# Kernel tuning notes

Measured on AMD Instinct MI355X. Metric: run time of the kernel, lower is better.

Reference implementation:

```python
import jax, jax.numpy as jnp
import numpy as np

M = 16                      # multiplicity of each irrep block
INV3 = 1.0 / np.sqrt(3.0)   # w3j(1,1,0) component-normalized
INV2 = 1.0 / np.sqrt(2.0)   # w3j(1,1,1) component-normalized
A0 = 1.0 / np.sqrt(2.0 * M) # fan-in norm for 0e outputs (2 paths x mul 16)
A1 = 1.0 / np.sqrt(3.0 * M) # fan-in norm for 1o outputs (3 paths x mul 16)


def setup_inputs() -> dict:
    E, N, ED, HID = 100000, 10000, 32, 128
    WNUM = 2 * M * (2 * M) + 3 * M * M  # 1792 per-edge TP weights
    ks = jax.random.split(jax.random.key(0), 10)
    return {
        "dst": jax.random.randint(ks[0], (E,), 0, N),
        "x_src": jax.random.normal(ks[1], (E, 4 * M), jnp.float32),   # 16x0e+16x1o
        "x_dst": jax.random.normal(ks[2], (N, 4 * M), jnp.float32),
        "sh": jax.random.normal(ks[3], (E, 4), jnp.float32),          # 1x0e+1x1o
        "edge_attr": jax.random.normal(ks[4], (E, ED), jnp.float32),
        "We1": jax.random.normal(ks[5], (ED, HID), jnp.float32) / np.sqrt(ED),
        "be1": jnp.zeros((HID,), jnp.float32),
        "We2": jax.random.normal(ks[6], (HID, WNUM), jnp.float32) / np.sqrt(HID),
        "be2": jnp.zeros((WNUM,), jnp.float32),
        "Wr0": jax.random.normal(ks[7], (M, 2 * M), jnp.float32),     # 16x0e -> 32x0e
        "Wr1": jax.random.normal(ks[8], (M, M), jnp.float32),         # 16x1o -> 16x1o
    }


def _forward(dst, x_src, x_dst, sh, edge_attr, We1, be1, We2, be2, Wr0, Wr1):
    E = x_src.shape[0]
    N = x_dst.shape[0]
    o0 = 2 * M  # 32x0e tp output (scalars + gates)

    # edge MLP -> per-edge tensor-product weights [E, 1792]
    w = jax.nn.relu(edge_attr @ We1 + be1) @ We2 + be2
    i = 0
    w_ss = w[:, i:i + M * o0].reshape(E, M, o0); i += M * o0   # 0e x 0e -> 0e
    w_vv0 = w[:, i:i + M * o0].reshape(E, M, o0); i += M * o0  # 1o x 1o -> 0e
    w_sv = w[:, i:i + M * M].reshape(E, M, M); i += M * M      # 0e x 1o -> 1o
    w_vs = w[:, i:i + M * M].reshape(E, M, M); i += M * M      # 1o x 0e -> 1o
    w_vv1 = w[:, i:i + M * M].reshape(E, M, M)                 # 1o x 1o -> 1o

    s1 = x_src[:, :M]                       # [E, 16]
    v1 = x_src[:, M:].reshape(E, M, 3)      # [E, 16, 3]
    s2 = sh[:, 0]                           # [E]
    v2 = sh[:, 1:4]                         # [E, 3]

    # fully-connected tensor product with per-edge weights
    out0 = A0 * (jnp.einsum('em,emo->eo', s1 * s2[:, None], w_ss)
                 + INV3 * jnp.einsum('emc,ec,emo->eo', v1, v2, w_vv0))  # [E, 32]
    cross = jnp.cross(v1, v2[:, None, :])   # [E, 16, 3]
    out1 = A1 * (jnp.einsum('em,ec,emo->eoc', s1, v2, w_sv)
                 + jnp.einsum('emc,e,emo->eoc', v1, s2, w_vs)
                 + INV2 * jnp.einsum('emc,emo->eoc', cross, w_vv1))     # [E, 16, 3]
    msg = jnp.concatenate([out0, out1.reshape(E, -1)], axis=1)          # [E, 80]

    # scatter-mean over destination nodes
    ssum = jax.ops.segment_sum(msg, dst, num_segments=N)
    cnt = jax.ops.segment_sum(jnp.ones((E,), msg.dtype), dst, num_segments=N)
    msg = ssum / jnp.maximum(cnt, 1.0)[:, None]                          # [N, 80]

    # residual equivariant linear on x_dst
    sd = x_dst[:, :M]
    vd = x_dst[:, M:].reshape(N, M, 3)
    res0 = (sd @ Wr0) / np.sqrt(M)                                       # [N, 32]
    res1 = jnp.einsum('nmc,mo->noc', vd, Wr1) / np.sqrt(M)               # [N, 16, 3]
    msg = msg + jnp.concatenate([res0, res1.reshape(N, -1)], axis=1)

    # gate nonlinearity: relu(scalars), sigmoid(gates) * gated vectors
    scalars = jax.nn.relu(msg[:, :M])
    gates = jax.nn.sigmoid(msg[:, M:2 * M])
    gated = msg[:, 2 * M:].reshape(N, M, 3) * gates[:, :, None]
    return jnp.concatenate([scalars, gated.reshape(N, -1)], axis=1)      # [N, 64]


def reference(dst, x_src, x_dst, sh, edge_attr, We1, be1, We2, be2, Wr0, Wr1):
    return _forward(dst, x_src, x_dst, sh, edge_attr, We1, be1, We2, be2, Wr0, Wr1)
```

## Files before the change

### kernel.cpp

```cpp
#include <hip/hip_runtime.h>
#include <math.h>

#define WNUM 1792
#define HID 128

#define INV3C 0.5773502691896258f
#define INV2C 0.7071067811865476f
#define A0C   0.17677669529663687f
#define A1C   0.14433756729740643f
#define MAXDEG 64

typedef short bf8 __attribute__((ext_vector_type(8)));
typedef _Float16 f16x8 __attribute__((ext_vector_type(8)));
typedef _Float16 f16x4 __attribute__((ext_vector_type(4)));
typedef float f32x4 __attribute__((ext_vector_type(4)));

__device__ inline unsigned short f2bf(float f) {
  union { float f; unsigned u; } v; v.f = f;
  unsigned r = v.u + 0x7FFFu + ((v.u >> 16) & 1u);
  return (unsigned short)(r >> 16);
}
__device__ inline float bf2f(unsigned short h) {
  union { unsigned u; float f; } v; v.u = ((unsigned)h) << 16;
  return v.f;
}
__device__ inline float wscale(int t) {
  if (t < 32) return A0C;
  if (t < 64) return A0C * INV3C;
  if (t < 96) return A1C;
  return A1C * INV2C;
}

__global__ __launch_bounds__(256) void prep_kernel(
    const float* __restrict__ We1, const float* __restrict__ We2,
    const float* __restrict__ be2,
    unsigned short* __restrict__ we1x, _Float16* __restrict__ we2h,
    float* __restrict__ be2p, int* __restrict__ cntp, int N)
{
  int i = blockIdx.x * 256 + threadIdx.x;
  if (i < 28672) {
    int t = i >> 8, c = (i >> 6) & 3, lane = i & 63;
    int quad = lane >> 4, l15 = lane & 15;
    int col = t * 16 + l15;
    float sc = wscale(t);
    f16x8 v;
    #pragma unroll
    for (int j = 0; j < 8; ++j) {
      int k = c * 32 + quad * 8 + j;
      v[j] = (_Float16)(We2[(size_t)k * WNUM + col] * sc);
    }
    *(f16x8*)(we2h + (size_t)t * 2048 + c * 512 + lane * 8) = v;
  } else if (i < 29184) {
    int q = i - 28672;
    int c1 = q >> 6, lane = q & 63;
    int quad = lane >> 4, l15 = lane & 15;
    int col = c1 * 16 + l15;
    bf8 hh, ll;
    #pragma unroll
    for (int j = 0; j < 8; ++j) {
      int k = quad * 8 + j;
      float v = We1[k * HID + col];
      unsigned short hi = f2bf(v);
      hh[j] = (short)hi;
      ll[j] = (short)f2bf(v - bf2f(hi));
    }
    *(bf8*)(we1x + c1 * 1024 + lane * 8) = hh;
    *(bf8*)(we1x + c1 * 1024 + 512 + lane * 8) = ll;
  } else if (i < 30976) {
    int q = i - 29184;
    int t = q >> 4, l16 = q & 15;
    be2p[(t >> 1) * 32 + l16 * 2 + (t & 1)] = be2[q] * wscale(t);
  } else if (i < 30976 + N) {
    cntp[i - 30976] = 0;
  }
}

__device__ inline void chains2(const f16x8* a0, const f16x8* a1,
    f16x8 b0, f16x8 b1, f16x8 b2, f16x8 b3,
    f16x8 b4, f16x8 b5, f16x8 b6, f16x8 b7,
    float2 bias, f32x4* wa, f32x4* wb)
{
  f32x4 ca0 = {bias.x, bias.x, bias.x, bias.x};
  f32x4 cb0 = {bias.y, bias.y, bias.y, bias.y};
  f32x4 ca1 = ca0, cb1 = cb0;
  ca0 = __builtin_amdgcn_mfma_f32_16x16x32_f16(a0[0], b0, ca0, 0, 0, 0);
  cb0 = __builtin_amdgcn_mfma_f32_16x16x32_f16(a0[0], b4, cb0, 0, 0, 0);
  ca1 = __builtin_amdgcn_mfma_f32_16x16x32_f16(a1[0], b0, ca1, 0, 0, 0);
  cb1 = __builtin_amdgcn_mfma_f32_16x16x32_f16(a1[0], b4, cb1, 0, 0, 0);
  ca0 = __builtin_amdgcn_mfma_f32_16x16x32_f16(a0[1], b1, ca0, 0, 0, 0);
  cb0 = __builtin_amdgcn_mfma_f32_16x16x32_f16(a0[1], b5, cb0, 0, 0, 0);
  ca1 = __builtin_amdgcn_mfma_f32_16x16x32_f16(a1[1], b1, ca1, 0, 0, 0);
  cb1 = __builtin_amdgcn_mfma_f32_16x16x32_f16(a1[1], b5, cb1, 0, 0, 0);
  ca0 = __builtin_amdgcn_mfma_f32_16x16x32_f16(a0[2], b2, ca0, 0, 0, 0);
  cb0 = __builtin_amdgcn_mfma_f32_16x16x32_f16(a0[2], b6, cb0, 0, 0, 0);
  ca1 = __builtin_amdgcn_mfma_f32_16x16x32_f16(a1[2], b2, ca1, 0, 0, 0);
  cb1 = __builtin_amdgcn_mfma_f32_16x16x32_f16(a1[2], b6, cb1, 0, 0, 0);
  ca0 = __builtin_amdgcn_mfma_f32_16x16x32_f16(a0[3], b3, ca0, 0, 0, 0);
  cb0 = __builtin_amdgcn_mfma_f32_16x16x32_f16(a0[3], b7, cb0, 0, 0, 0);
  ca1 = __builtin_amdgcn_mfma_f32_16x16x32_f16(a1[3], b3, ca1, 0, 0, 0);
  cb1 = __builtin_amdgcn_mfma_f32_16x16x32_f16(a1[3], b7, cb1, 0, 0, 0);
  wa[0] = ca0; wb[0] = cb0; wa[1] = ca1; wb[1] = cb1;
}

__device__ inline void pair_mm(const _Float16* bL, const float* bp, int p,
                               const f16x8 (&af)[2][4], f32x4* wa, f32x4* wb)
{
  f16x8 b0 = *(const f16x8*)(bL);
  f16x8 b1 = *(const f16x8*)(bL + 512);
  f16x8 b2 = *(const f16x8*)(bL + 1024);
  f16x8 b3 = *(const f16x8*)(bL + 1536);
  f16x8 b4 = *(const f16x8*)(bL + 2048);
  f16x8 b5 = *(const f16x8*)(bL + 2560);
  f16x8 b6 = *(const f16x8*)(bL + 3072);
  f16x8 b7 = *(const f16x8*)(bL + 3584);
  float2 bias2 = *(const float2*)(bp + p * 32);
  chains2(af[0], af[1], b0, b1, b2, b3, b4, b5, b6, b7, bias2, wa, wb);
}

template <bool MSG>
__global__ __launch_bounds__(256, 2) void edge_kernel(
    const float* __restrict__ ea, const float* __restrict__ xsrc,
    const float* __restrict__ sh, const int* __restrict__ dst,
    const float* __restrict__ be1,
    const unsigned short* __restrict__ we1x, const _Float16* __restrict__ we2h,
    const float* __restrict__ be2p,
    float* __restrict__ outp, int* __restrict__ eidx, int* __restrict__ cntp, int E)
{
  const int lane = threadIdx.x & 63;
  const int w    = threadIdx.x >> 6;
  const int quad = lane >> 4;
  const int l16  = lane & 15;
  const int eb   = (blockIdx.x * 4 + w) * 32;

  __shared__ union SMem {
    _Float16 h[4][32][136];
    _Float16 B[4][4096];
  } uS;
  __shared__ _Float16 fss_s[4][16][32];
  __shared__ _Float16 fvv_s[4][16][32];
  __shared__ _Float16 s1h_s[4][16][32];
  __shared__ _Float16 v1h_s[4][16][3][32];
  __shared__ float4 vq_s[4][32];

  #define STAGE_PAIR(p) { \
    const _Float16* gsrc_ = we2h + (size_t)(p) * 4096; \
    _Float16* ldst_ = &uS.B[(p) & 3][0]; \
    __builtin_amdgcn_global_load_lds( \
      (const __attribute__((address_space(1))) void*)(gsrc_ + (w * 2) * 512 + lane * 8), \
      (__attribute__((address_space(3))) void*)(ldst_ + (w * 2) * 512), 16, 0, 0); \
    __builtin_amdgcn_global_load_lds( \
      (const __attribute__((address_space(1))) void*)(gsrc_ + (w * 2 + 1) * 512 + lane * 8), \
      (__attribute__((address_space(3))) void*)(ldst_ + (w * 2 + 1) * 512), 16, 0, 0); \
  }

  if (lane < 32) {
    int ge = eb + lane;
    if (ge < E) {
      int node = dst[ge];
      int pos = atomicAdd(cntp + node, 1);
      if (MSG) { if (pos < MAXDEG) eidx[node * MAXDEG + pos] = ge; }
    }
  }

  {
    int e2 = lane >> 1, mg = lane & 1;
    int ge = eb + e2;
    if (ge < E) {
      const float* xp = xsrc + (size_t)ge * 64;
      float4 sq0 = *(const float4*)(xp + mg * 8);
      float4 sq1 = *(const float4*)(xp + mg * 8 + 4);
      float s1a[8] = {sq0.x,sq0.y,sq0.z,sq0.w,sq1.x,sq1.y,sq1.z,sq1.w};
      const float* vp = xp + 16 + mg * 24;
      float la[24];
      #pragma unroll
      for (int qv = 0; qv < 6; ++qv) {
        float4 t = *(const float4*)(vp + qv * 4);
        la[qv*4+0] = t.x; la[qv*4+1] = t.y; la[qv*4+2] = t.z; la[qv*4+3] = t.w;
      }
      float4 shq = *(const float4*)(sh + (size_t)ge * 4);
      float s2 = shq.x, v2x = shq.y, v2y = shq.z, v2z = shq.w;
      #pragma unroll
      for (int mi = 0; mi < 8; ++mi) {
        int m = mg * 8 + mi;
        float v1x = la[mi*3], v1y = la[mi*3+1], v1z = la[mi*3+2];
        fss_s[w][m][e2] = (_Float16)(s1a[mi] * s2);
        fvv_s[w][m][e2] = (_Float16)(v1x*v2x + v1y*v2y + v1z*v2z);
        s1h_s[w][m][e2] = (_Float16)s1a[mi];
        v1h_s[w][m][0][e2] = (_Float16)v1x;
        v1h_s[w][m][1][e2] = (_Float16)v1y;
        v1h_s[w][m][2][e2] = (_Float16)v1z;
      }
      if (mg == 0) vq_s[w][e2] = make_float4(v2x, v2y, v2z, s2);
    } else {
      #pragma unroll
      for (int mi = 0; mi < 8; ++mi) {
        int m = mg * 8 + mi;
        fss_s[w][m][e2] = (_Float16)0.f;
        fvv_s[w][m][e2] = (_Float16)0.f;
        s1h_s[w][m][e2] = (_Float16)0.f;
        v1h_s[w][m][0][e2] = (_Float16)0.f;
        v1h_s[w][m][1][e2] = (_Float16)0.f;
        v1h_s[w][m][2][e2] = (_Float16)0.f;
      }
      if (mg == 0) vq_s[w][e2] = make_float4(0,0,0,0);
    }
  }

  {
    bf8 ah[2], al[2];
    #pragma unroll
    for (int g = 0; g < 2; ++g) {
      int gea = eb + g * 16 + l16; if (gea > E - 1) gea = E - 1;
      const float* ep = ea + (size_t)gea * 32 + quad * 8;
      float4 p0 = *(const float4*)ep;
      float4 p1 = *(const float4*)(ep + 4);
      float pv[8] = {p0.x,p0.y,p0.z,p0.w,p1.x,p1.y,p1.z,p1.w};
      #pragma unroll
      for (int j = 0; j < 8; ++j) {
        unsigned short hi = f2bf(pv[j]);
        ah[g][j] = (short)hi;
        al[g][j] = (short)f2bf(pv[j] - bf2f(hi));
      }
    }
    const unsigned short* wb1 = we1x + lane * 8;
    #pragma unroll 2
    for (int c = 0; c < 8; ++c) {
      bf8 bh = *(const bf8*)(wb1 + c * 1024);
      bf8 bl = *(const bf8*)(wb1 + c * 1024 + 512);
      float bias = be1[c * 16 + l16];
      #pragma unroll
      for (int g = 0; g < 2; ++g) {
        f32x4 hc = {bias, bias, bias, bias};
        hc = __builtin_amdgcn_mfma_f32_16x16x32_bf16(al[g], bh, hc, 0, 0, 0);
        hc = __builtin_amdgcn_mfma_f32_16x16x32_bf16(ah[g], bl, hc, 0, 0, 0);
        hc = __builtin_amdgcn_mfma_f32_16x16x32_bf16(ah[g], bh, hc, 0, 0, 0);
        #pragma unroll
        for (int r = 0; r < 4; ++r)
          uS.h[w][g * 16 + quad * 4 + r][c * 16 + l16] = (_Float16)fmaxf(hc[r], 0.f);
      }
    }
  }
  __syncthreads();

  f16x8 af[2][4];
  #pragma unroll
  for (int g = 0; g < 2; ++g)
    #pragma unroll
    for (int ch = 0; ch < 4; ++ch)
      af[g][ch] = *(const f16x8*)&uS.h[w][g * 16 + l16][ch * 32 + quad * 8];
  __syncthreads();

  STAGE_PAIR(0)
  STAGE_PAIR(1)
  __syncthreads();

  const float* bp = be2p + l16 * 2;
  float m0a[2][4] = {{0,0,0,0},{0,0,0,0}}, m0b[2][4] = {{0,0,0,0},{0,0,0,0}};

  #pragma unroll 1
  for (int i = 0; i < 16; i += 2) {
    STAGE_PAIR(i + 2)
    STAGE_PAIR(i + 3)
    f32x4 wa[2], wb[2];
    pair_mm(&uS.B[i & 3][lane * 8], bp, i, af, wa, wb);
    #pragma unroll
    for (int g = 0; g < 2; ++g) {
      f16x4 fv = *(const f16x4*)&fss_s[w][i][g * 16 + quad * 4];
      #pragma unroll
      for (int r = 0; r < 4; ++r) {
        float f = (float)fv[r];
        m0a[g][r] = fmaf(wa[g][r], f, m0a[g][r]);
        m0b[g][r] = fmaf(wb[g][r], f, m0b[g][r]);
      }
    }
    pair_mm(&uS.B[(i + 1) & 3][lane * 8], bp, i + 1, af, wa, wb);
    #pragma unroll
    for (int g = 0; g < 2; ++g) {
      f16x4 fv = *(const f16x4*)&fss_s[w][i + 1][g * 16 + quad * 4];
      #pragma unroll
      for (int r = 0; r < 4; ++r) {
        float f = (float)fv[r];
        m0a[g][r] = fmaf(wa[g][r], f, m0a[g][r]);
        m0b[g][r] = fmaf(wb[g][r], f, m0b[g][r]);
      }
    }
    __syncthreads();
  }

  #pragma unroll 1
  for (int i = 0; i < 16; i += 2) {
    int pg = 16 + i;
    STAGE_PAIR(pg + 2)
    STAGE_PAIR(pg + 3)
    f32x4 wa[2], wb[2];
    pair_mm(&uS.B[pg & 3][lane * 8], bp, pg, af, wa, wb);
    #pragma unroll
    for (int g = 0; g < 2; ++g) {
      f16x4 fv = *(const f16x4*)&fvv_s[w][i][g * 16 + quad * 4];
      #pragma unroll
      for (int r = 0; r < 4; ++r) {
        float f = (float)fv[r];
        m0a[g][r] = fmaf(wa[g][r], f, m0a[g][r]);
        m0b[g][r] = fmaf(wb[g][r], f, m0b[g][r]);
      }
    }
    pair_mm(&uS.B[(pg + 1) & 3][lane * 8], bp, pg + 1, af, wa, wb);
    #pragma unroll
    for (int g = 0; g < 2; ++g) {
      f16x4 fv = *(const f16x4*)&fvv_s[w][i + 1][g * 16 + quad * 4];
      #pragma unroll
      for (int r = 0; r < 4; ++r) {
        float f = (float)fv[r];
        m0a[g][r] = fmaf(wa[g][r], f, m0a[g][r]);
        m0b[g][r] = fmaf(wb[g][r], f, m0b[g][r]);
      }
    }
    __syncthreads();
  }

  #pragma unroll
  for (int g = 0; g < 2; ++g)
    #pragma unroll
    for (int r = 0; r < 4; ++r) {
      int ge = eb + g * 16 + quad * 4 + r;
      if (ge < E) {
        if (MSG) {
          float* mp = outp + (size_t)ge * 80;
          mp[l16]      = m0a[g][r];
          mp[16 + l16] = m0b[g][r];
        } else {
          float* ap = outp + (size_t)dst[ge] * 80;
          atomicAdd(ap + l16,      m0a[g][r]);
          atomicAdd(ap + 16 + l16, m0b[g][r]);
        }
      }
    }

  float sg[2][4] = {{0,0,0,0},{0,0,0,0}};
  #pragma unroll 1
  for (int i = 0; i < 8; i += 2) {
    int pg = 32 + i;
    STAGE_PAIR(pg + 2)
    STAGE_PAIR(pg + 3)
    f32x4 wa[2], wb[2];
    pair_mm(&uS.B[pg & 3][lane * 8], bp, pg, af, wa, wb);
    #pragma unroll
    for (int g = 0; g < 2; ++g) {
      f16x4 sA = *(const f16x4*)&s1h_s[w][2*i][g * 16 + quad * 4];
      f16x4 sB = *(const f16x4*)&s1h_s[w][2*i + 1][g * 16 + quad * 4];
      #pragma unroll
      for (int r = 0; r < 4; ++r)
        sg[g][r] = fmaf(wb[g][r], (float)sB[r], fmaf(wa[g][r], (float)sA[r], sg[g][r]));
    }
    pair_mm(&uS.B[(pg + 1) & 3][lane * 8], bp, pg + 1, af, wa, wb);
    #pragma unroll
    for (int g = 0; g < 2; ++g) {
      f16x4 sA = *(const f16x4*)&s1h_s[w][2*i + 2][g * 16 + quad * 4];
      f16x4 sB = *(const f16x4*)&s1h_s[w][2*i + 3][g * 16 + quad * 4];
      #pragma unroll
      for (int r = 0; r < 4; ++r)
        sg[g][r] = fmaf(wb[g][r], (float)sB[r], fmaf(wa[g][r], (float)sA[r], sg[g][r]));
    }
    __syncthreads();
  }
  float4 vq[2][4];
  #pragma unroll
  for (int g = 0; g < 2; ++g)
    #pragma unroll
    for (int r = 0; r < 4; ++r) vq[g][r] = vq_s[w][g * 16 + quad * 4 + r];

  float m1x[2][4], m1y[2][4], m1z[2][4];
  #pragma unroll
  for (int g = 0; g < 2; ++g)
    #pragma unroll
    for (int r = 0; r < 4; ++r) {
      m1x[g][r] = sg[g][r] * vq[g][r].x;
      m1y[g][r] = sg[g][r] * vq[g][r].y;
      m1z[g][r] = sg[g][r] * vq[g][r].z;
    }

  #pragma unroll
  for (int sec = 0; sec < 2; ++sec) {
    float ux[2][4] = {{0,0,0,0},{0,0,0,0}}, uy[2][4] = {{0,0,0,0},{0,0,0,0}},
          uz[2][4] = {{0,0,0,0},{0,0,0,0}};
    int base = 40 + sec * 8;
    #pragma unroll 1
    for (int i = 0; i < 8; i += 2) {
      int pg = base + i;
      if (pg + 2 < 56) STAGE_PAIR(pg + 2)
      if (pg + 3 < 56) STAGE_PAIR(pg + 3)
      f32x4 wa[2], wb[2];
      pair_mm(&uS.B[pg & 3][lane * 8], bp, pg, af, wa, wb);
      #pragma unroll
      for (int g = 0; g < 2; ++g) {
        f16x4 xA = *(const f16x4*)&v1h_s[w][2*i][0][g*16 + quad*4];
        f16x4 xB = *(const f16x4*)&v1h_s[w][2*i+1][0][g*16 + quad*4];
        f16x4 yA = *(const f16x4*)&v1h_s[w][2*i][1][g*16 + quad*4];
        f16x4 yB = *(const f16x4*)&v1h_s[w][2*i+1][1][g*16 + quad*4];
        f16x4 zA = *(const f16x4*)&v1h_s[w][2*i][2][g*16 + quad*4];
        f16x4 zB = *(const f16x4*)&v1h_s[w][2*i+1][2][g*16 + quad*4];
        #pragma unroll
        for (int r = 0; r < 4; ++r) {
          ux[g][r] = fmaf(wb[g][r], (float)xB[r], fmaf(wa[g][r], (float)xA[r], ux[g][r]));
          uy[g][r] = fmaf(wb[g][r], (float)yB[r], fmaf(wa[g][r], (float)yA[r], uy[g][r]));
          uz[g][r] = fmaf(wb[g][r], (float)zB[r], fmaf(wa[g][r], (float)zA[r], uz[g][r]));
        }
      }
      pair_mm(&uS.B[(pg + 1) & 3][lane * 8], bp, pg + 1, af, wa, wb);
      #pragma unroll
      for (int g = 0; g < 2; ++g) {
        f16x4 xA = *(const f16x4*)&v1h_s[w][2*i+2][0][g*16 + quad*4];
        f16x4 xB = *(const f16x4*)&v1h_s[w][2*i+3][0][g*16 + quad*4];
        f16x4 yA = *(const f16x4*)&v1h_s[w][2*i+2][1][g*16 + quad*4];
        f16x4 yB = *(const f16x4*)&v1h_s[w][2*i+3][1][g*16 + quad*4];
        f16x4 zA = *(const f16x4*)&v1h_s[w][2*i+2][2][g*16 + quad*4];
        f16x4 zB = *(const f16x4*)&v1h_s[w][2*i+3][2][g*16 + quad*4];
        #pragma unroll
        for (int r = 0; r < 4; ++r) {
          ux[g][r] = fmaf(wb[g][r], (float)xB[r], fmaf(wa[g][r], (float)xA[r], ux[g][r]));
          uy[g][r] = fmaf(wb[g][r], (float)yB[r], fmaf(wa[g][r], (float)yA[r], uy[g][r]));
          uz[g][r] = fmaf(wb[g][r], (float)zB[r], fmaf(wa[g][r], (float)zA[r], uz[g][r]));
        }
      }
      __syncthreads();
    }
    if (sec == 0) {
      #pragma unroll
      for (int g = 0; g < 2; ++g)
        #pragma unroll
        for (int r = 0; r < 4; ++r) {
          m1x[g][r] = fmaf(vq[g][r].w, ux[g][r], m1x[g][r]);
          m1y[g][r] = fmaf(vq[g][r].w, uy[g][r], m1y[g][r]);
          m1z[g][r] = fmaf(vq[g][r].w, uz[g][r], m1z[g][r]);
        }
    } else {
      #pragma unroll
      for (int g = 0; g < 2; ++g)
        #pragma unroll
        for (int r = 0; r < 4; ++r) {
          m1x[g][r] = fmaf(uy[g][r], vq[g][r].z, m1x[g][r]);
          m1x[g][r] = fmaf(-uz[g][r], vq[g][r].y, m1x[g][r]);
          m1y[g][r] = fmaf(uz[g][r], vq[g][r].x, m1y[g][r]);
          m1y[g][r] = fmaf(-ux[g][r], vq[g][r].z, m1y[g][r]);
          m1z[g][r] = fmaf(ux[g][r], vq[g][r].y, m1z[g][r]);
          m1z[g][r] = fmaf(-uy[g][r], vq[g][r].x, m1z[g][r]);
        }
    }
  }

  #pragma unroll
  for (int g = 0; g < 2; ++g)
    #pragma unroll
    for (int r = 0; r < 4; ++r) {
      int ge = eb + g * 16 + quad * 4 + r;
      if (ge < E) {
        if (MSG) {
          float* mp = outp + (size_t)ge * 80;
          mp[32 + l16*3 + 0] = m1x[g][r];
          mp[32 + l16*3 + 1] = m1y[g][r];
          mp[32 + l16*3 + 2] = m1z[g][r];
        } else {
          float* ap = outp + (size_t)dst[ge] * 80;
          atomicAdd(ap + 32 + l16*3 + 0, m1x[g][r]);
          atomicAdd(ap + 32 + l16*3 + 1, m1y[g][r]);
          atomicAdd(ap + 32 + l16*3 + 2, m1z[g][r]);
        }
      }
    }
  #undef STAGE_PAIR
}

__global__ __launch_bounds__(128) void node_gather_kernel(
    const float* __restrict__ msg, const int* __restrict__ eidx,
    const int* __restrict__ cntp,
    const float* __restrict__ xdst, const float* __restrict__ Wr0,
    const float* __restrict__ Wr1, float* __restrict__ out, int N)
{
  int n = blockIdx.x;
  if (n >= N) return;
  int j = threadIdx.x;
  int c0 = cntp[n];
  int deg = c0 < MAXDEG ? c0 : MAXDEG;
  float inv = 1.0f / fmaxf((float)c0, 1.0f);
  __shared__ float s_sum[80];
  if (j < 80) {
    float s = 0.f;
    const int* ep = eidx + (size_t)n * MAXDEG;
    int i = 0;
    for (; i + 1 < deg; i += 2) {
      int e0 = ep[i], e1 = ep[i + 1];
      s += msg[(size_t)e0 * 80 + j] + msg[(size_t)e1 * 80 + j];
    }
    if (i < deg) s += msg[(size_t)ep[i] * 80 + j];
    s_sum[j] = s * inv;
  }
  __syncthreads();
  if (j >= 64) return;
  const float* xd = xdst + (size_t)n * 64;
  float* op = out + (size_t)n * 64;
  if (j < 16) {
    float s = 0.f;
    #pragma unroll
    for (int m = 0; m < 16; ++m) s = fmaf(xd[m], Wr0[m * 32 + j], s);
    op[j] = fmaxf(s_sum[j] + 0.25f * s, 0.f);
  } else {
    int jj = j - 16;
    int o = (jj * 86) >> 8;
    int c = jj - o * 3;
    float tg = 0.f, v = 0.f;
    #pragma unroll
    for (int m = 0; m < 16; ++m) {
      tg = fmaf(xd[m], Wr0[m * 32 + 16 + o], tg);
      v  = fmaf(xd[16 + m * 3 + c], Wr1[m * 16 + o], v);
    }
    float g = 1.0f / (1.0f + expf(-(s_sum[16 + o] + 0.25f * tg)));
    op[16 + jj] = (s_sum[32 + jj] + 0.25f * v) * g;
  }
}

__global__ __launch_bounds__(256) void node_kernel(
    const float* __restrict__ accn, const int* __restrict__ cntp,
    const float* __restrict__ xdst, const float* __restrict__ Wr0,
    const float* __restrict__ Wr1, float* __restrict__ out, int N)
{
  int idx = blockIdx.x * 256 + threadIdx.x;
  int n = idx >> 6, j = idx & 63;
  if (n >= N) return;
  float inv = 1.0f / fmaxf((float)cntp[n], 1.0f);
  const float* ap = accn + (size_t)n * 80;
  const float* xd = xdst + (size_t)n * 64;
  float* op = out + (size_t)n * 64;
  if (j < 16) {
    float s = 0.f;
    #pragma unroll
    for (int m = 0; m < 16; ++m) s = fmaf(xd[m], Wr0[m * 32 + j], s);
    op[j] = fmaxf(ap[j] * inv + 0.25f * s, 0.f);
  } else {
    int jj = j - 16;
    int o = (jj * 86) >> 8;
    int c = jj - o * 3;
    float tg = 0.f, v = 0.f;
    #pragma unroll
    for (int m = 0; m < 16; ++m) {
      tg = fmaf(xd[m], Wr0[m * 32 + 16 + o], tg);
      v  = fmaf(xd[16 + m * 3 + c], Wr1[m * 16 + o], v);
    }
    float g = 1.0f / (1.0f + expf(-(ap[16 + o] * inv + 0.25f * tg)));
    op[16 + jj] = (ap[32 + jj] * inv + 0.25f * v) * g;
  }
}

extern "C" void kernel_launch(void* const* d_in, const int* in_sizes, int n_in,
                              void* d_out, int out_size, void* d_ws, size_t ws_size,
                              hipStream_t stream)
{
  const int*   dst  = (const int*)d_in[0];
  const float* xsrc = (const float*)d_in[1];
  const float* xdst = (const float*)d_in[2];
  const float* sh   = (const float*)d_in[3];
  const float* ea   = (const float*)d_in[4];
  const float* We1  = (const float*)d_in[5];
  const float* be1  = (const float*)d_in[6];
  const float* We2  = (const float*)d_in[7];
  const float* be2  = (const float*)d_in[8];
  const float* Wr0  = (const float*)d_in[9];
  const float* Wr1  = (const float*)d_in[10];
  const int E = in_sizes[0];
  const int N = in_sizes[2] / 64;

  char* ws = (char*)d_ws;
  _Float16* we2h = (_Float16*)ws;
  unsigned short* we1x = (unsigned short*)(ws + 458752);
  float* be2p = (float*)(ws + 475136);
  int*   cntp = (int*)(ws + 482560);
  size_t off = 482560 + (size_t)N * 4;
  off = (off + 15) & ~(size_t)15;

  size_t need_msg = off + (size_t)N * MAXDEG * 4 + (size_t)E * 80 * 4;
  bool use_msg = (ws_size >= need_msg);

  prep_kernel<<<(30976 + N + 255) / 256, 256, 0, stream>>>(We1, We2, be2,
      we1x, we2h, be2p, cntp, N);

  if (use_msg) {
    int* eidx = (int*)(ws + off);
    float* msg = (float*)(ws + off + (size_t)N * MAXDEG * 4);
    edge_kernel<true><<<(E + 127) / 128, 256, 0, stream>>>(ea, xsrc, sh, dst, be1,
        we1x, we2h, be2p, msg, eidx, cntp, E);
    node_gather_kernel<<<N, 128, 0, stream>>>(msg, eidx, cntp, xdst, Wr0, Wr1,
        (float*)d_out, N);
  } else {
    float* accn = (float*)(ws + off);
    hipMemsetAsync(accn, 0, (size_t)N * 320, stream);
    edge_kernel<false><<<(E + 127) / 128, 256, 0, stream>>>(ea, xsrc, sh, dst, be1,
        we1x, we2h, be2p, accn, (int*)nullptr, cntp, E);
    node_kernel<<<((size_t)N * 64 + 255) / 256, 256, 0, stream>>>(accn, cntp,
        xdst, Wr0, Wr1, (float*)d_out, N);
  }
}
```

Baseline: 195.4 us.

## Drop precomputed fss/fvv LDS buffers and raise occupancy to three blocks

Removes the fss_s and fvv_s shared arrays. The s1*s2 and v1·v2 factors are now rebuilt inside the 0e-output loops from the existing s1h_s/v1h_s arrays and per-edge sh values cached in registers. This cuts LDS footprint, and the launch bound is raised from 2 to 3 blocks per CU to use the freed space for more resident blocks. The cost is extra LDS reads (three per vector step instead of one), extra FMAs, more live registers under a tighter register cap, and slightly different rounding because products are now formed in fp32 from fp16 inputs.

```diff
diff --git a/kernel.cpp b/kernel.cpp
--- a/kernel.cpp
+++ b/kernel.cpp
@@ -118,7 +118,7 @@
 }
 
 template <bool MSG>
-__global__ __launch_bounds__(256, 2) void edge_kernel(
+__global__ __launch_bounds__(256, 3) void edge_kernel(
     const float* __restrict__ ea, const float* __restrict__ xsrc,
     const float* __restrict__ sh, const int* __restrict__ dst,
     const float* __restrict__ be1,
@@ -136,8 +136,6 @@
     _Float16 h[4][32][136];
     _Float16 B[4][4096];
   } uS;
-  __shared__ _Float16 fss_s[4][16][32];
-  __shared__ _Float16 fvv_s[4][16][32];
   __shared__ _Float16 s1h_s[4][16][32];
   __shared__ _Float16 v1h_s[4][16][3][32];
   __shared__ float4 vq_s[4][32];
@@ -183,8 +181,6 @@
       for (int mi = 0; mi < 8; ++mi) {
         int m = mg * 8 + mi;
         float v1x = la[mi*3], v1y = la[mi*3+1], v1z = la[mi*3+2];
-        fss_s[w][m][e2] = (_Float16)(s1a[mi] * s2);
-        fvv_s[w][m][e2] = (_Float16)(v1x*v2x + v1y*v2y + v1z*v2z);
         s1h_s[w][m][e2] = (_Float16)s1a[mi];
         v1h_s[w][m][0][e2] = (_Float16)v1x;
         v1h_s[w][m][1][e2] = (_Float16)v1y;
@@ -195,8 +191,6 @@
       #pragma unroll
       for (int mi = 0; mi < 8; ++mi) {
         int m = mg * 8 + mi;
-        fss_s[w][m][e2] = (_Float16)0.f;
-        fvv_s[w][m][e2] = (_Float16)0.f;
         s1h_s[w][m][e2] = (_Float16)0.f;
         v1h_s[w][m][0][e2] = (_Float16)0.f;
         v1h_s[w][m][1][e2] = (_Float16)0.f;
@@ -257,6 +251,13 @@
   const float* bp = be2p + l16 * 2;
   float m0a[2][4] = {{0,0,0,0},{0,0,0,0}}, m0b[2][4] = {{0,0,0,0},{0,0,0,0}};
 
+  float s2v[2][4];
+  #pragma unroll
+  for (int g = 0; g < 2; ++g)
+    #pragma unroll
+    for (int r = 0; r < 4; ++r)
+      s2v[g][r] = vq_s[w][g * 16 + quad * 4 + r].w;
+
   #pragma unroll 1
   for (int i = 0; i < 16; i += 2) {
     STAGE_PAIR(i + 2)
@@ -265,10 +266,10 @@
     pair_mm(&uS.B[i & 3][lane * 8], bp, i, af, wa, wb);
     #pragma unroll
     for (int g = 0; g < 2; ++g) {
-      f16x4 fv = *(const f16x4*)&fss_s[w][i][g * 16 + quad * 4];
+      f16x4 fv = *(const f16x4*)&s1h_s[w][i][g * 16 + quad * 4];
       #pragma unroll
       for (int r = 0; r < 4; ++r) {
-        float f = (float)fv[r];
+        float f = (float)fv[r] * s2v[g][r];
         m0a[g][r] = fmaf(wa[g][r], f, m0a[g][r]);
         m0b[g][r] = fmaf(wb[g][r], f, m0b[g][r]);
       }
@@ -276,16 +277,25 @@
     pair_mm(&uS.B[(i + 1) & 3][lane * 8], bp, i + 1, af, wa, wb);
     #pragma unroll
     for (int g = 0; g < 2; ++g) {
-      f16x4 fv = *(const f16x4*)&fss_s[w][i + 1][g * 16 + quad * 4];
+      f16x4 fv = *(const f16x4*)&s1h_s[w][i + 1][g * 16 + quad * 4];
       #pragma unroll
       for (int r = 0; r < 4; ++r) {
-        float f = (float)fv[r];
+        float f = (float)fv[r] * s2v[g][r];
         m0a[g][r] = fmaf(wa[g][r], f, m0a[g][r]);
         m0b[g][r] = fmaf(wb[g][r], f, m0b[g][r]);
       }
     }
     __syncthreads();
   }
+
+  float v2xv[2][4], v2yv[2][4], v2zv[2][4];
+  #pragma unroll
+  for (int g = 0; g < 2; ++g)
+    #pragma unroll
+    for (int r = 0; r < 4; ++r) {
+      float4 q = vq_s[w][g * 16 + quad * 4 + r];
+      v2xv[g][r] = q.x; v2yv[g][r] = q.y; v2zv[g][r] = q.z;
+    }
 
   #pragma unroll 1
   for (int i = 0; i < 16; i += 2) {
@@ -296,10 +306,13 @@
     pair_mm(&uS.B[pg & 3][lane * 8], bp, pg, af, wa, wb);
     #pragma unroll
     for (int g = 0; g < 2; ++g) {
-      f16x4 fv = *(const f16x4*)&fvv_s[w][i][g * 16 + quad * 4];
+      f16x4 xA = *(const f16x4*)&v1h_s[w][i][0][g * 16 + quad * 4];
+      f16x4 yA = *(const f16x4*)&v1h_s[w][i][1][g * 16 + quad * 4];
+      f16x4 zA = *(const f16x4*)&v1h_s[w][i][2][g * 16 + quad * 4];
       #pragma unroll
       for (int r = 0; r < 4; ++r) {
-        float f = (float)fv[r];
+        float f = fmaf((float)zA[r], v2zv[g][r],
+                  fmaf((float)yA[r], v2yv[g][r], (float)xA[r] * v2xv[g][r]));
         m0a[g][r] = fmaf(wa[g][r], f, m0a[g][r]);
         m0b[g][r] = fmaf(wb[g][r], f, m0b[g][r]);
       }
@@ -307,10 +320,13 @@
     pair_mm(&uS.B[(pg + 1) & 3][lane * 8], bp, pg + 1, af, wa, wb);
     #pragma unroll
     for (int g = 0; g < 2; ++g) {
-      f16x4 fv = *(const f16x4*)&fvv_s[w][i + 1][g * 16 + quad * 4];
+      f16x4 xA = *(const f16x4*)&v1h_s[w][i + 1][0][g * 16 + quad * 4];
+      f16x4 yA = *(const f16x4*)&v1h_s[w][i + 1][1][g * 16 + quad * 4];
+      f16x4 zA = *(const f16x4*)&v1h_s[w][i + 1][2][g * 16 + quad * 4];
       #pragma unroll
       for (int r = 0; r < 4; ++r) {
-        float f = (float)fv[r];
+        float f = fmaf((float)zA[r], v2zv[g][r],
+                  fmaf((float)yA[r], v2yv[g][r], (float)xA[r] * v2xv[g][r]));
         m0a[g][r] = fmaf(wa[g][r], f, m0a[g][r]);
         m0b[g][r] = fmaf(wb[g][r], f, m0b[g][r]);
       }
```

Measured after the change: 239.3 us. 22.5% more time.
